# Optimization experiments

Measured on AMD Instinct MI355X. Metric: run time of the kernel, lower is better.

The kernel has to match this reference:

```python
import jax, jax.numpy as jnp
import numpy as np

B, T, NX, NXS, H, NY, NYS = 16384, 60, 4, 3, 64, 4, 3


def _lstm(x, h0, c0, Wih, Whh, bih, bhh):
    """PyTorch-convention LSTM (gate order i,f,g,o). x: [B,T,X]. Returns (hs [B,T,H], hT, cT)."""
    # precompute input contribution for all timesteps: [T,B,4H]
    xg = jnp.transpose(jnp.einsum('btx,gx->btg', x, Wih) + (bih + bhh), (1, 0, 2))

    def step(carry, xg_t):
        h, c = carry
        g = xg_t + h @ Whh.T
        i, f, gg, o = jnp.split(g, 4, axis=-1)
        c = jax.nn.sigmoid(f) * c + jax.nn.sigmoid(i) * jnp.tanh(gg)
        h = jax.nn.sigmoid(o) * jnp.tanh(c)
        return (h, c), h

    (hT, cT), hs = jax.lax.scan(step, (h0, c0), xg)
    return jnp.transpose(hs, (1, 0, 2)), hT, cT


def setup_inputs() -> dict:
    key = jax.random.key(0)
    ks = jax.random.split(key, 24)
    w = lambda k, shp: (jax.random.normal(k, shp, jnp.float32) * 0.1)
    return {
        'inputs_main': jax.random.normal(ks[0], (B, T, NX), jnp.float32),
        'inputs_aux': jax.random.normal(ks[1], (B, NXS), jnp.float32),
        'hx2': jax.random.normal(ks[2], (B, H), jnp.float32),
        'cx2': jax.random.normal(ks[3], (B, H), jnp.float32),
        'Ws1': w(ks[4], (H, NXS)), 'bs1': w(ks[5], (H,)),
        'Ws2': w(ks[6], (H, NXS)), 'bs2': w(ks[7], (H,)),
        'Wih1': w(ks[8], (4 * H, NX)), 'Whh1': w(ks[9], (4 * H, H)),
        'bih1': w(ks[10], (4 * H,)), 'bhh1': w(ks[11], (4 * H,)),
        'Wih2': w(ks[12], (4 * H, H)), 'Whh2': w(ks[13], (4 * H, H)),
        'bih2': w(ks[14], (4 * H,)), 'bhh2': w(ks[15], (4 * H,)),
        'Wlat': w(ks[16], (H, H)), 'blat': w(ks[17], (H,)),
        'Wout': w(ks[18], (NY, H)), 'bout': w(ks[19], (NY,)),
        'Wsfc': w(ks[20], (NYS, H)), 'bsfc': w(ks[21], (NYS,)),
    }


def reference(inputs_main, inputs_aux, hx2, cx2, Ws1, bs1, Ws2, bs2,
              Wih1, Whh1, bih1, bhh1, Wih2, Whh2, bih2, bhh2,
              Wlat, blat, Wout, bout, Wsfc, bsfc):
    # surface MLPs -> initial LSTM1 state (h raw, c tanh'd)
    hx = inputs_aux @ Ws1.T + bs1
    cx = jnp.tanh(inputs_aux @ Ws2.T + bs2)
    # run LSTM1 top-down (flipped levels)
    x1 = jnp.flip(inputs_main, axis=1)
    rnn1out, _, _ = _lstm(x1, hx, cx, Wih1, Whh1, bih1, bhh1)
    # flip back and run LSTM2 bottom-up with (hx2, cx2)
    # (the original calls rnn2 twice; only the second call's result is used)
    rnn1out_f = jnp.flip(rnn1out, axis=1)
    rnn2out, last_h, _ = _lstm(rnn1out_f, hx2, cx2, Wih2, Whh2, bih2, bhh2)
    # intermediate MLP + output head
    lat = rnn2out @ Wlat.T + blat                # [B,T,H]
    out = lat @ Wout.T + bout                    # [B,T,NY]
    out_sfc = jax.nn.relu(last_h @ Wsfc.T + bsfc)  # [B,NYS]
    return out, out_sfc
```

## Files before the change

### kernel.cpp

```cpp
#include <hip/hip_runtime.h>
#include <hip/hip_bf16.h>

#define BB 16384
#define TT 60

typedef short bf16x8 __attribute__((ext_vector_type(8)));
typedef float f32x4 __attribute__((ext_vector_type(4)));

__device__ __forceinline__ unsigned short f2bs(float f) {
    __hip_bfloat16 h = __float2bfloat16(f);
    return __builtin_bit_cast(unsigned short, h);
}

__device__ __forceinline__ unsigned cvtpk2(float lo, float hi) {
    unsigned r;
    asm("v_cvt_pk_bf16_f32 %0, %1, %2" : "=v"(r) : "v"(lo), "v"(hi));
    return r;
}

__device__ __forceinline__ void lstm_cell(float xi, float xf, float xg, float xo,
                                          float& c, float& h) {
    xi = __builtin_amdgcn_fmed3f(xi, -17.f, 17.f);
    xf = __builtin_amdgcn_fmed3f(xf, -17.f, 17.f);
    xo = __builtin_amdgcn_fmed3f(xo, -17.f, 17.f);
    xg = __builtin_amdgcn_fmed3f(xg, -11.f, 11.f);
    const float ei = __expf(-xi), ef = __expf(-xf), eo = __expf(-xo), eg = __expf(2.f * xg);
    const float di = 1.f + ei, df = 1.f + ef, dd = 1.f + eo, dg = 1.f + eg;
    const float a = di * df, b = dd * dg;
    const float R = __builtin_amdgcn_rcpf(a * b);
    const float si = df * b * R;
    const float sf = di * b * R;
    const float so = a * dg * R;
    const float tg = (eg - 1.f) * (a * dd) * R;
    const float cn = sf * c + si * tg;
    c = cn;
    const float tc = __builtin_amdgcn_fmed3f(cn, -11.f, 11.f);
    const float ec = __expf(2.f * tc);
    const float th = (ec - 1.f) * __builtin_amdgcn_rcpf(ec + 1.f);
    h = so * th;
}

#define STEP_BARRIER() do {                                   \
    asm volatile("s_waitcnt lgkmcnt(0)" ::: "memory");        \
    __builtin_amdgcn_s_barrier();                             \
    __builtin_amdgcn_sched_barrier(0);                        \
} while (0)

__device__ __forceinline__ bf16x8 pack8(float4 a, float4 b) {
    bf16x8 r;
    r[0] = (short)f2bs(a.x); r[1] = (short)f2bs(a.y);
    r[2] = (short)f2bs(a.z); r[3] = (short)f2bs(a.w);
    r[4] = (short)f2bs(b.x); r[5] = (short)f2bs(b.y);
    r[6] = (short)f2bs(b.z); r[7] = (short)f2bs(b.w);
    return r;
}

__global__ __launch_bounds__(256, 2) void k_lstm1(
    const float* __restrict__ xmain, const float* __restrict__ aux,
    const float* __restrict__ Ws1, const float* __restrict__ bs1,
    const float* __restrict__ Ws2, const float* __restrict__ bs2,
    const float* __restrict__ Wih1, const float* __restrict__ Whh1,
    const float* __restrict__ bih1, const float* __restrict__ bhh1,
    unsigned short* __restrict__ rnn1t)
{
    __shared__ unsigned short hB[2 * 4096];

    const int tid = threadIdx.x;
    {
        unsigned int* p32 = (unsigned int*)hB;
        #pragma unroll
        for (int e = 0; e < 16; ++e) p32[tid + 256 * e] = 0;
    }
    const int hj = tid >> 6, lane = tid & 63;
    const int row16 = lane & 15, quad = lane >> 4;
    const int b0 = blockIdx.x * 32;
    const int swz = (row16 & 7) << 3;

    bf16x8 wf[4][3];
    float fb[4];
    #pragma unroll
    for (int i = 0; i < 4; ++i) {
        const int g = (hj + 4 * i) * 16 + row16;
        const float* wr = Whh1 + g * 64 + quad * 8;
        wf[i][0] = pack8(*(const float4*)wr, *(const float4*)(wr + 4));
        wf[i][1] = pack8(*(const float4*)(wr + 32), *(const float4*)(wr + 36));
        float4 z4 = {0.f, 0.f, 0.f, 0.f};
        float4 xw = z4;
        if (quad == 0) xw = *(const float4*)(Wih1 + g * 4);
        wf[i][2] = pack8(xw, z4);
        fb[i] = bih1[g] + bhh1[g];
    }
    __syncthreads();

    const int j = hj * 16 + row16;
    const unsigned oA0 = (unsigned)(((row16 * 128 + 0 + quad * 8) ^ swz) * 2);
    const unsigned oA1 = (unsigned)(((row16 * 128 + 32 + quad * 8) ^ swz) * 2);
    const unsigned oA2 = (unsigned)(((row16 * 128 + 64 + quad * 8) ^ swz) * 2);
    unsigned oW[4];
    #pragma unroll
    for (int r = 0; r < 4; ++r) {
        const int m = quad * 4 + r;
        oW[r] = (unsigned)(((m * 128 + j) ^ ((m & 7) << 3)) * 2);
    }
    const unsigned oX = (unsigned)(((lane * 128 + 64) ^ ((lane & 7) << 3)) * 2);
    char* const hBb = (char*)hB;

    const float w10 = Ws1[j * 3], w11 = Ws1[j * 3 + 1], w12 = Ws1[j * 3 + 2], sb1v = bs1[j];
    const float w20 = Ws2[j * 3], w21 = Ws2[j * 3 + 1], w22 = Ws2[j * 3 + 2], sb2v = bs2[j];
    f32x4 cc[2];
    #pragma unroll
    for (int mh = 0; mh < 2; ++mh) {
        #pragma unroll
        for (int r = 0; r < 4; ++r) {
            const int m = mh * 16 + quad * 4 + r;
            const float a0v = aux[(b0 + m) * 3], a1v = aux[(b0 + m) * 3 + 1], a2v = aux[(b0 + m) * 3 + 2];
            float h0 = w10 * a0v + w11 * a1v + w12 * a2v + sb1v;
            float c0in = w20 * a0v + w21 * a1v + w22 * a2v + sb2v;
            c0in = __builtin_amdgcn_fmed3f(c0in, -11.f, 11.f);
            const float e0 = __expf(2.f * c0in);
            cc[mh][r] = (e0 - 1.f) * __builtin_amdgcn_rcpf(e0 + 1.f);
            *(unsigned short*)(hBb + oW[r] + mh * 4096) = f2bs(h0);
        }
    }
    if (hj == 2 && lane < 32) {
        float4 xv = ((const float4*)xmain)[(size_t)(b0 + lane) * TT + 59];
        uint2 p2 = { cvtpk2(xv.x, xv.y), cvtpk2(xv.z, xv.w) };
        *(uint2*)(hBb + oX) = p2;
    }
    __syncthreads();

    const float4* px = (const float4*)xmain + (size_t)(b0 + lane) * TT + 58;
    unsigned short* pst = rnn1t + ((size_t)60 * BB + b0 + ((hj >> 1) << 4) + row16) * 64 + ((hj & 1) << 5) + quad * 8;

    unsigned pofs = 0;
    #pragma unroll 1
    for (int s = 0; s < TT; ++s) {
        char* hbP = hBb + pofs;
        char* hbN = hBb + (pofs ^ 8192);
        float4 xv;
        if (hj == 2 && lane < 32 && s < TT - 1) xv = *px;
        bf16x8 a0[2], a1[2], a2[2];
        #pragma unroll
        for (int mh = 0; mh < 2; ++mh) {
            a0[mh] = *(const bf16x8*)(hbP + oA0 + mh * 4096);
            a1[mh] = *(const bf16x8*)(hbP + oA1 + mh * 4096);
            a2[mh] = *(const bf16x8*)(hbP + oA2 + mh * 4096);
        }
        if (s > 0) {
            bf16x8 sv = (hj == 0) ? a0[0] : (hj == 1) ? a1[0] : (hj == 2) ? a0[1] : a1[1];
            *(bf16x8*)pst = sv;
        }
        pst -= (size_t)BB * 64;
        px -= 1;

        f32x4 ac[2][4];
        #pragma unroll
        for (int mh = 0; mh < 2; ++mh)
            #pragma unroll
            for (int i = 0; i < 4; ++i) { f32x4 v = {fb[i], fb[i], fb[i], fb[i]}; ac[mh][i] = v; }
        #pragma unroll
        for (int mh = 0; mh < 2; ++mh) {
            #pragma unroll
            for (int i = 0; i < 4; ++i) {
                ac[mh][i] = __builtin_amdgcn_mfma_f32_16x16x32_bf16(a0[mh], wf[i][0], ac[mh][i], 0, 0, 0);
                ac[mh][i] = __builtin_amdgcn_mfma_f32_16x16x32_bf16(a1[mh], wf[i][1], ac[mh][i], 0, 0, 0);
                ac[mh][i] = __builtin_amdgcn_mfma_f32_16x16x32_bf16(a2[mh], wf[i][2], ac[mh][i], 0, 0, 0);
            }
        }
        #pragma unroll
        for (int mh = 0; mh < 2; ++mh) {
            float hr[4];
            #pragma unroll
            for (int r = 0; r < 4; ++r) {
                float cr = cc[mh][r];
                lstm_cell(ac[mh][0][r], ac[mh][1][r], ac[mh][2][r], ac[mh][3][r], cr, hr[r]);
                cc[mh][r] = cr;
            }
            const unsigned u01 = cvtpk2(hr[0], hr[1]);
            const unsigned u23 = cvtpk2(hr[2], hr[3]);
            *(unsigned short*)(hbN + oW[0] + mh * 4096) = (unsigned short)u01;
            *(unsigned short*)(hbN + oW[1] + mh * 4096) = (unsigned short)(u01 >> 16);
            *(unsigned short*)(hbN + oW[2] + mh * 4096) = (unsigned short)u23;
            *(unsigned short*)(hbN + oW[3] + mh * 4096) = (unsigned short)(u23 >> 16);
        }
        if (hj == 2 && lane < 32 && s < TT - 1) {
            uint2 p2 = { cvtpk2(xv.x, xv.y), cvtpk2(xv.z, xv.w) };
            *(uint2*)(hbN + oX) = p2;
        }
        STEP_BARRIER();
        pofs ^= 8192;
    }
    {
        char* hbP = hBb + pofs;
        bf16x8 sv;
        if (hj == 0)      sv = *(const bf16x8*)(hbP + oA0);
        else if (hj == 1) sv = *(const bf16x8*)(hbP + oA1);
        else if (hj == 2) sv = *(const bf16x8*)(hbP + oA0 + 4096);
        else              sv = *(const bf16x8*)(hbP + oA1 + 4096);
        *(bf16x8*)&rnn1t[((size_t)(b0 + ((hj >> 1) << 4) + row16)) * 64 + ((hj & 1) << 5) + quad * 8] = sv;
    }
}

__global__ __launch_bounds__(256, 2) void k_lstm2(
    const unsigned short* __restrict__ rnn1t,
    const float* __restrict__ hx2, const float* __restrict__ cx2,
    const float* __restrict__ Wih2, const float* __restrict__ Whh2,
    const float* __restrict__ bih2, const float* __restrict__ bhh2,
    const float* __restrict__ Wlat, const float* __restrict__ blat,
    const float* __restrict__ Wout, const float* __restrict__ bout,
    const float* __restrict__ Wsfc, const float* __restrict__ bsfc,
    float* __restrict__ out)
{
    __shared__ unsigned short hB[2 * 4096];
    __shared__ unsigned short whead[16 * 64];

    const int tid = threadIdx.x;
    {
        unsigned int* w32 = (unsigned int*)whead;
        w32[tid] = 0; w32[tid + 256] = 0;
    }
    const int hj = tid >> 6, lane = tid & 63;
    const int row16 = lane & 15, quad = lane >> 4;
    const int b0 = blockIdx.x * 32;
    const int swz = (row16 & 7) << 3;

    bf16x8 wf[4][4];
    float fb[4];
    #pragma unroll
    for (int i = 0; i < 4; ++i) {
        const int g = (hj + 4 * i) * 16 + row16;
        const float* wh = Whh2 + g * 64 + quad * 8;
        const float* wi = Wih2 + g * 64 + quad * 8;
        wf[i][0] = pack8(*(const float4*)wh, *(const float4*)(wh + 4));
        wf[i][1] = pack8(*(const float4*)(wh + 32), *(const float4*)(wh + 36));
        wf[i][2] = pack8(*(const float4*)wi, *(const float4*)(wi + 4));
        wf[i][3] = pack8(*(const float4*)(wi + 32), *(const float4*)(wi + 36));
        fb[i] = bih2[g] + bhh2[g];
    }
    float bcomb = 0.f;
    if (row16 < 4) {
        float s = 0.f;
        for (int jj = 0; jj < 64; ++jj) s += Wout[row16 * 64 + jj] * blat[jj];
        bcomb = s + bout[row16];
    } else if (row16 < 7) {
        bcomb = bsfc[row16 - 4];
    }
    __syncthreads();

    {
        const int o = tid >> 6, k = tid & 63;
        float s = 0.f;
        for (int jj = 0; jj < 64; ++jj) s += Wout[o * 64 + jj] * Wlat[jj * 64 + k];
        whead[(o * 64 + k) ^ ((o & 7) << 3)] = f2bs(s);
        if (tid < 192) {
            const int o2 = o + 4;
            whead[(o2 * 64 + k) ^ ((o2 & 7) << 3)] = f2bs(Wsfc[o * 64 + k]);
        }
    }

    const int j = hj * 16 + row16;
    const unsigned oA0 = (unsigned)(((row16 * 128 + 0 + quad * 8) ^ swz) * 2);
    const unsigned oA1 = (unsigned)(((row16 * 128 + 32 + quad * 8) ^ swz) * 2);
    const unsigned oA2 = (unsigned)(((row16 * 128 + 64 + quad * 8) ^ swz) * 2);
    const unsigned oA3 = (unsigned)(((row16 * 128 + 96 + quad * 8) ^ swz) * 2);
    unsigned oW[4];
    #pragma unroll
    for (int r = 0; r < 4; ++r) {
        const int m = quad * 4 + r;
        oW[r] = (unsigned)(((m * 128 + j) ^ ((m & 7) << 3)) * 2);
    }
    const unsigned oPV = (unsigned)(((row16 * 128 + 64 + ((hj & 1) << 5) + quad * 8) ^ swz) * 2);
    const unsigned oH0 = (unsigned)(((row16 * 64 + 0 + quad * 8) ^ swz) * 2);
    const unsigned oH1 = (unsigned)(((row16 * 64 + 32 + quad * 8) ^ swz) * 2);
    char* const hBb = (char*)hB;
    char* const whb = (char*)whead;

    f32x4 cc[2];
    #pragma unroll
    for (int mh = 0; mh < 2; ++mh) {
        #pragma unroll
        for (int r = 0; r < 4; ++r) {
            const int m = mh * 16 + quad * 4 + r;
            cc[mh][r] = cx2[(size_t)(b0 + m) * 64 + j];
            *(unsigned short*)(hBb + oW[r] + mh * 4096) = f2bs(hx2[(size_t)(b0 + m) * 64 + j]);
        }
    }
    if (hj < 2) {
        bf16x8 v0 = *(const bf16x8*)&rnn1t[((size_t)(b0 + row16)) * 64 + ((hj & 1) << 5) + quad * 8];
        bf16x8 v1 = *(const bf16x8*)&rnn1t[((size_t)(b0 + 16 + row16)) * 64 + ((hj & 1) << 5) + quad * 8];
        *(bf16x8*)(hBb + oPV) = v0;
        *(bf16x8*)(hBb + oPV + 4096) = v1;
    }
    __syncthreads();

    bf16x8 wh0 = *(const bf16x8*)(whb + oH0);
    bf16x8 wh1 = *(const bf16x8*)(whb + oH1);

    const unsigned short* ppv = rnn1t + ((size_t)BB + b0 + row16) * 64 + ((hj & 1) << 5) + quad * 8;
    float* po = out + ((size_t)(b0 + ((hj == 2) ? 16 : 0) + quad * 4) * TT) * 4 + row16;

    unsigned pofs = 0;
    #pragma unroll 1
    for (int t = 0; t < TT; ++t) {
        char* hbP = hBb + pofs;
        char* hbN = hBb + (pofs ^ 8192);
        bf16x8 pv0, pv1;
        if (hj < 2 && t < TT - 1) {
            pv0 = *(const bf16x8*)ppv;
            pv1 = *(const bf16x8*)(ppv + 16 * 64);
        }
        ppv += (size_t)BB * 64;

        bf16x8 a0[2], a1[2], a2[2], a3[2];
        #pragma unroll
        for (int mh = 0; mh < 2; ++mh) {
            a0[mh] = *(const bf16x8*)(hbP + oA0 + mh * 4096);
            a1[mh] = *(const bf16x8*)(hbP + oA1 + mh * 4096);
            a2[mh] = *(const bf16x8*)(hbP + oA2 + mh * 4096);
            a3[mh] = *(const bf16x8*)(hbP + oA3 + mh * 4096);
        }

        if (hj >= 2 && t > 0) {
            const bf16x8 ha0 = (hj == 3) ? a0[0] : a0[1];
            const bf16x8 ha1 = (hj == 3) ? a1[0] : a1[1];
            f32x4 hacc = {bcomb, bcomb, bcomb, bcomb};
            hacc = __builtin_amdgcn_mfma_f32_16x16x32_bf16(ha0, wh0, hacc, 0, 0, 0);
            hacc = __builtin_amdgcn_mfma_f32_16x16x32_bf16(ha1, wh1, hacc, 0, 0, 0);
            if (row16 < 4) {
                #pragma unroll
                for (int r = 0; r < 4; ++r)
                    po[r * TT * 4] = hacc[r];
            }
            po += 4;
        }

        f32x4 ac[2][4];
        #pragma unroll
        for (int mh = 0; mh < 2; ++mh)
            #pragma unroll
            for (int i = 0; i < 4; ++i) { f32x4 v = {fb[i], fb[i], fb[i], fb[i]}; ac[mh][i] = v; }
        #pragma unroll
        for (int mh = 0; mh < 2; ++mh) {
            #pragma unroll
            for (int i = 0; i < 4; ++i) {
                ac[mh][i] = __builtin_amdgcn_mfma_f32_16x16x32_bf16(a0[mh], wf[i][0], ac[mh][i], 0, 0, 0);
                ac[mh][i] = __builtin_amdgcn_mfma_f32_16x16x32_bf16(a1[mh], wf[i][1], ac[mh][i], 0, 0, 0);
                ac[mh][i] = __builtin_amdgcn_mfma_f32_16x16x32_bf16(a2[mh], wf[i][2], ac[mh][i], 0, 0, 0);
                ac[mh][i] = __builtin_amdgcn_mfma_f32_16x16x32_bf16(a3[mh], wf[i][3], ac[mh][i], 0, 0, 0);
            }
        }
        #pragma unroll
        for (int mh = 0; mh < 2; ++mh) {
            float hr[4];
            #pragma unroll
            for (int r = 0; r < 4; ++r) {
                float cr = cc[mh][r];
                lstm_cell(ac[mh][0][r], ac[mh][1][r], ac[mh][2][r], ac[mh][3][r], cr, hr[r]);
                cc[mh][r] = cr;
            }
            const unsigned u01 = cvtpk2(hr[0], hr[1]);
            const unsigned u23 = cvtpk2(hr[2], hr[3]);
            *(unsigned short*)(hbN + oW[0] + mh * 4096) = (unsigned short)u01;
            *(unsigned short*)(hbN + oW[1] + mh * 4096) = (unsigned short)(u01 >> 16);
            *(unsigned short*)(hbN + oW[2] + mh * 4096) = (unsigned short)u23;
            *(unsigned short*)(hbN + oW[3] + mh * 4096) = (unsigned short)(u23 >> 16);
        }
        if (hj < 2 && t < TT - 1) {
            *(bf16x8*)(hbN + oPV) = pv0;
            *(bf16x8*)(hbN + oPV + 4096) = pv1;
        }
        STEP_BARRIER();
        pofs ^= 8192;
    }
    if (hj >= 2) {
        char* hbP = hBb + pofs;
        const int mho = (hj == 3) ? 0 : 4096;
        bf16x8 ea0 = *(const bf16x8*)(hbP + oA0 + mho);
        bf16x8 ea1 = *(const bf16x8*)(hbP + oA1 + mho);
        f32x4 hacc = {bcomb, bcomb, bcomb, bcomb};
        hacc = __builtin_amdgcn_mfma_f32_16x16x32_bf16(ea0, wh0, hacc, 0, 0, 0);
        hacc = __builtin_amdgcn_mfma_f32_16x16x32_bf16(ea1, wh1, hacc, 0, 0, 0);
        const int rb = b0 + ((hj == 2) ? 16 : 0) + quad * 4;
        if (row16 < 4) {
            #pragma unroll
            for (int r = 0; r < 4; ++r)
                out[((size_t)(rb + r) * TT + 59) * 4 + row16] = hacc[r];
        } else if (row16 < 7) {
            float* osfc = out + (size_t)BB * TT * 4;
            #pragma unroll
            for (int r = 0; r < 4; ++r)
                osfc[(size_t)(rb + r) * 3 + (row16 - 4)] = fmaxf(hacc[r], 0.f);
        }
    }
}

extern "C" void kernel_launch(void* const* d_in, const int* in_sizes, int n_in,
                              void* d_out, int out_size, void* d_ws, size_t ws_size,
                              hipStream_t stream) {
    const float* xmain = (const float*)d_in[0];
    const float* aux   = (const float*)d_in[1];
    const float* hx2   = (const float*)d_in[2];
    const float* cx2   = (const float*)d_in[3];
    const float* Ws1   = (const float*)d_in[4];
    const float* bs1   = (const float*)d_in[5];
    const float* Ws2   = (const float*)d_in[6];
    const float* bs2   = (const float*)d_in[7];
    const float* Wih1  = (const float*)d_in[8];
    const float* Whh1  = (const float*)d_in[9];
    const float* bih1  = (const float*)d_in[10];
    const float* bhh1  = (const float*)d_in[11];
    const float* Wih2  = (const float*)d_in[12];
    const float* Whh2  = (const float*)d_in[13];
    const float* bih2  = (const float*)d_in[14];
    const float* bhh2  = (const float*)d_in[15];
    const float* Wlat  = (const float*)d_in[16];
    const float* blat  = (const float*)d_in[17];
    const float* Wout  = (const float*)d_in[18];
    const float* bout  = (const float*)d_in[19];
    const float* Wsfc  = (const float*)d_in[20];
    const float* bsfc  = (const float*)d_in[21];

    unsigned short* rnn1t = (unsigned short*)d_ws;
    float* out = (float*)d_out;

    dim3 grid(BB / 32), block(256);
    k_lstm1<<<grid, block, 0, stream>>>(xmain, aux, Ws1, bs1, Ws2, bs2,
                                        Wih1, Whh1, bih1, bhh1, rnn1t);
    k_lstm2<<<grid, block, 0, stream>>>(rnn1t, hx2, cx2, Wih2, Whh2, bih2, bhh2,
                                        Wlat, blat, Wout, bout, Wsfc, bsfc, out);
}
```

Before: 237.6 us.

## Fold exp2 scaling into LSTM weights and split LSTM2 h/x LDS buffers

Multiplies the recurrent and input weights and biases by -log2(e) (or 2·log2(e) for the g gate) at load time, so the cell can call exp2 directly without negating or scaling the pre-activations. The clamp bounds are rescaled to match. In LSTM2, the shared h-state buffer is split into separate h2 and h1 buffers, and every wave now prefetches one rnn1 row-slice per step instead of two waves each loading two. The m-half loop is also made non-unrolled, which lowers register pressure but serialises MFMA and activation work across the two halves. Folding the scale into bf16 weights shifts rounding slightly.

```diff
diff --git a/kernel.cpp b/kernel.cpp
--- a/kernel.cpp
+++ b/kernel.cpp
@@ -3,6 +3,7 @@
 
 #define BB 16384
 #define TT 60
+#define L2E 1.44269504089f
 
 typedef short bf16x8 __attribute__((ext_vector_type(8)));
 typedef float f32x4 __attribute__((ext_vector_type(4)));
@@ -18,13 +19,14 @@
     return r;
 }
 
-__device__ __forceinline__ void lstm_cell(float xi, float xf, float xg, float xo,
+__device__ __forceinline__ void lstm_cell(float yi, float yf, float yg, float yo,
                                           float& c, float& h) {
-    xi = __builtin_amdgcn_fmed3f(xi, -17.f, 17.f);
-    xf = __builtin_amdgcn_fmed3f(xf, -17.f, 17.f);
-    xo = __builtin_amdgcn_fmed3f(xo, -17.f, 17.f);
-    xg = __builtin_amdgcn_fmed3f(xg, -11.f, 11.f);
-    const float ei = __expf(-xi), ef = __expf(-xf), eo = __expf(-xo), eg = __expf(2.f * xg);
+    yi = __builtin_amdgcn_fmed3f(yi, -24.53f, 24.53f);
+    yf = __builtin_amdgcn_fmed3f(yf, -24.53f, 24.53f);
+    yo = __builtin_amdgcn_fmed3f(yo, -24.53f, 24.53f);
+    yg = __builtin_amdgcn_fmed3f(yg, -31.74f, 31.74f);
+    const float ei = __builtin_exp2f(yi), ef = __builtin_exp2f(yf);
+    const float eo = __builtin_exp2f(yo), eg = __builtin_exp2f(yg);
     const float di = 1.f + ei, df = 1.f + ef, dd = 1.f + eo, dg = 1.f + eg;
     const float a = di * df, b = dd * dg;
     const float R = __builtin_amdgcn_rcpf(a * b);
@@ -35,7 +37,7 @@
     const float cn = sf * c + si * tg;
     c = cn;
     const float tc = __builtin_amdgcn_fmed3f(cn, -11.f, 11.f);
-    const float ec = __expf(2.f * tc);
+    const float ec = __builtin_exp2f(2.f * L2E * tc);
     const float th = (ec - 1.f) * __builtin_amdgcn_rcpf(ec + 1.f);
     h = so * th;
 }
@@ -46,12 +48,12 @@
     __builtin_amdgcn_sched_barrier(0);                        \
 } while (0)
 
-__device__ __forceinline__ bf16x8 pack8(float4 a, float4 b) {
+__device__ __forceinline__ bf16x8 pack8s(float4 a, float4 b, float s) {
     bf16x8 r;
-    r[0] = (short)f2bs(a.x); r[1] = (short)f2bs(a.y);
-    r[2] = (short)f2bs(a.z); r[3] = (short)f2bs(a.w);
-    r[4] = (short)f2bs(b.x); r[5] = (short)f2bs(b.y);
-    r[6] = (short)f2bs(b.z); r[7] = (short)f2bs(b.w);
+    r[0] = (short)f2bs(a.x * s); r[1] = (short)f2bs(a.y * s);
+    r[2] = (short)f2bs(a.z * s); r[3] = (short)f2bs(a.w * s);
+    r[4] = (short)f2bs(b.x * s); r[5] = (short)f2bs(b.y * s);
+    r[6] = (short)f2bs(b.z * s); r[7] = (short)f2bs(b.w * s);
     return r;
 }
 
@@ -76,19 +78,22 @@
     const int b0 = blockIdx.x * 32;
     const int swz = (row16 & 7) << 3;
 
+    const float gs = (hj == 2) ? (2.f * L2E) : (-L2E);
+    (void)gs;
     bf16x8 wf[4][3];
     float fb[4];
     #pragma unroll
     for (int i = 0; i < 4; ++i) {
+        const float s = (i == 2) ? (2.f * L2E) : (-L2E);
         const int g = (hj + 4 * i) * 16 + row16;
         const float* wr = Whh1 + g * 64 + quad * 8;
-        wf[i][0] = pack8(*(const float4*)wr, *(const float4*)(wr + 4));
-        wf[i][1] = pack8(*(const float4*)(wr + 32), *(const float4*)(wr + 36));
+        wf[i][0] = pack8s(*(const float4*)wr, *(const float4*)(wr + 4), s);
+        wf[i][1] = pack8s(*(const float4*)(wr + 32), *(const float4*)(wr + 36), s);
         float4 z4 = {0.f, 0.f, 0.f, 0.f};
         float4 xw = z4;
         if (quad == 0) xw = *(const float4*)(Wih1 + g * 4);
-        wf[i][2] = pack8(xw, z4);
-        fb[i] = bih1[g] + bhh1[g];
+        wf[i][2] = pack8s(xw, z4, s);
+        fb[i] = (bih1[g] + bhh1[g]) * s;
     }
     __syncthreads();
 
@@ -117,7 +122,7 @@
             float h0 = w10 * a0v + w11 * a1v + w12 * a2v + sb1v;
             float c0in = w20 * a0v + w21 * a1v + w22 * a2v + sb2v;
             c0in = __builtin_amdgcn_fmed3f(c0in, -11.f, 11.f);
-            const float e0 = __expf(2.f * c0in);
+            const float e0 = __builtin_exp2f(2.f * L2E * c0in);
             cc[mh][r] = (e0 - 1.f) * __builtin_amdgcn_rcpf(e0 + 1.f);
             *(unsigned short*)(hBb + oW[r] + mh * 4096) = f2bs(h0);
         }
@@ -211,7 +216,8 @@
     const float* __restrict__ Wsfc, const float* __restrict__ bsfc,
     float* __restrict__ out)
 {
-    __shared__ unsigned short hB[2 * 4096];
+    __shared__ unsigned short h2B[2 * 2048];
+    __shared__ unsigned short h1B[2 * 2048];
     __shared__ unsigned short whead[16 * 64];
 
     const int tid = threadIdx.x;
@@ -228,20 +234,21 @@
     float fb[4];
     #pragma unroll
     for (int i = 0; i < 4; ++i) {
+        const float s = (i == 2) ? (2.f * L2E) : (-L2E);
         const int g = (hj + 4 * i) * 16 + row16;
         const float* wh = Whh2 + g * 64 + quad * 8;
         const float* wi = Wih2 + g * 64 + quad * 8;
-        wf[i][0] = pack8(*(const float4*)wh, *(const float4*)(wh + 4));
-        wf[i][1] = pack8(*(const float4*)(wh + 32), *(const float4*)(wh + 36));
-        wf[i][2] = pack8(*(const float4*)wi, *(const float4*)(wi + 4));
-        wf[i][3] = pack8(*(const float4*)(wi + 32), *(const float4*)(wi + 36));
-        fb[i] = bih2[g] + bhh2[g];
+        wf[i][0] = pack8s(*(const float4*)wh, *(const float4*)(wh + 4), s);
+        wf[i][1] = pack8s(*(const float4*)(wh + 32), *(const float4*)(wh + 36), s);
+        wf[i][2] = pack8s(*(const float4*)wi, *(const float4*)(wi + 4), s);
+        wf[i][3] = pack8s(*(const float4*)(wi + 32), *(const float4*)(wi + 36), s);
+        fb[i] = (bih2[g] + bhh2[g]) * s;
     }
     float bcomb = 0.f;
     if (row16 < 4) {
-        float s = 0.f;
-        for (int jj = 0; jj < 64; ++jj) s += Wout[row16 * 64 + jj] * blat[jj];
-        bcomb = s + bout[row16];
+        float ss = 0.f;
+        for (int jj = 0; jj < 64; ++jj) ss += Wout[row16 * 64 + jj] * blat[jj];
+        bcomb = ss + bout[row16];
     } else if (row16 < 7) {
         bcomb = bsfc[row16 - 4];
     }
@@ -249,9 +256,9 @@
 
     {
         const int o = tid >> 6, k = tid & 63;
-        float s = 0.f;
-        for (int jj = 0; jj < 64; ++jj) s += Wout[o * 64 + jj] * Wlat[jj * 64 + k];
-        whead[(o * 64 + k) ^ ((o & 7) << 3)] = f2bs(s);
+        float ss = 0.f;
+        for (int jj = 0; jj < 64; ++jj) ss += Wout[o * 64 + jj] * Wlat[jj * 64 + k];
+        whead[(o * 64 + k) ^ ((o & 7) << 3)] = f2bs(ss);
         if (tid < 192) {
             const int o2 = o + 4;
             whead[(o2 * 64 + k) ^ ((o2 & 7) << 3)] = f2bs(Wsfc[o * 64 + k]);
@@ -259,20 +266,19 @@
     }
 
     const int j = hj * 16 + row16;
-    const unsigned oA0 = (unsigned)(((row16 * 128 + 0 + quad * 8) ^ swz) * 2);
-    const unsigned oA1 = (unsigned)(((row16 * 128 + 32 + quad * 8) ^ swz) * 2);
-    const unsigned oA2 = (unsigned)(((row16 * 128 + 64 + quad * 8) ^ swz) * 2);
-    const unsigned oA3 = (unsigned)(((row16 * 128 + 96 + quad * 8) ^ swz) * 2);
+    const unsigned oA0 = (unsigned)(((row16 * 64 + 0 + quad * 8) ^ swz) * 2);
+    const unsigned oA1 = (unsigned)(((row16 * 64 + 32 + quad * 8) ^ swz) * 2);
     unsigned oW[4];
     #pragma unroll
     for (int r = 0; r < 4; ++r) {
         const int m = quad * 4 + r;
-        oW[r] = (unsigned)(((m * 128 + j) ^ ((m & 7) << 3)) * 2);
-    }
-    const unsigned oPV = (unsigned)(((row16 * 128 + 64 + ((hj & 1) << 5) + quad * 8) ^ swz) * 2);
+        oW[r] = (unsigned)(((m * 64 + j) ^ ((m & 7) << 3)) * 2);
+    }
+    const unsigned oPV = (unsigned)((hj >> 1) * 2048 + (((row16 * 64 + ((hj & 1) << 5) + quad * 8) ^ swz) * 2));
     const unsigned oH0 = (unsigned)(((row16 * 64 + 0 + quad * 8) ^ swz) * 2);
     const unsigned oH1 = (unsigned)(((row16 * 64 + 32 + quad * 8) ^ swz) * 2);
-    char* const hBb = (char*)hB;
+    char* const h2Bb = (char*)h2B;
+    char* const h1Bb = (char*)h1B;
     char* const whb = (char*)whead;
 
     f32x4 cc[2];
@@ -282,101 +288,86 @@
         for (int r = 0; r < 4; ++r) {
             const int m = mh * 16 + quad * 4 + r;
             cc[mh][r] = cx2[(size_t)(b0 + m) * 64 + j];
-            *(unsigned short*)(hBb + oW[r] + mh * 4096) = f2bs(hx2[(size_t)(b0 + m) * 64 + j]);
-        }
-    }
-    if (hj < 2) {
-        bf16x8 v0 = *(const bf16x8*)&rnn1t[((size_t)(b0 + row16)) * 64 + ((hj & 1) << 5) + quad * 8];
-        bf16x8 v1 = *(const bf16x8*)&rnn1t[((size_t)(b0 + 16 + row16)) * 64 + ((hj & 1) << 5) + quad * 8];
-        *(bf16x8*)(hBb + oPV) = v0;
-        *(bf16x8*)(hBb + oPV + 4096) = v1;
+            *(unsigned short*)(h2Bb + oW[r] + mh * 2048) = f2bs(hx2[(size_t)(b0 + m) * 64 + j]);
+        }
+    }
+    const unsigned short* pbase = rnn1t + ((size_t)(b0 + ((hj >> 1) << 4) + row16)) * 64 + ((hj & 1) << 5) + quad * 8;
+    {
+        bf16x8 v = *(const bf16x8*)pbase;
+        *(bf16x8*)(h1Bb + oPV) = v;
     }
     __syncthreads();
 
     bf16x8 wh0 = *(const bf16x8*)(whb + oH0);
     bf16x8 wh1 = *(const bf16x8*)(whb + oH1);
 
-    const unsigned short* ppv = rnn1t + ((size_t)BB + b0 + row16) * 64 + ((hj & 1) << 5) + quad * 8;
+    const unsigned short* ppv = pbase + (size_t)BB * 64;
     float* po = out + ((size_t)(b0 + ((hj == 2) ? 16 : 0) + quad * 4) * TT) * 4 + row16;
 
     unsigned pofs = 0;
     #pragma unroll 1
     for (int t = 0; t < TT; ++t) {
-        char* hbP = hBb + pofs;
-        char* hbN = hBb + (pofs ^ 8192);
-        bf16x8 pv0, pv1;
-        if (hj < 2 && t < TT - 1) {
-            pv0 = *(const bf16x8*)ppv;
-            pv1 = *(const bf16x8*)(ppv + 16 * 64);
-        }
+        char* hbP2 = h2Bb + pofs;
+        char* hbN2 = h2Bb + (pofs ^ 4096);
+        char* hbP1 = h1Bb + pofs;
+        char* hbN1 = h1Bb + (pofs ^ 4096);
+        bf16x8 pv;
+        if (t < TT - 1) pv = *(const bf16x8*)ppv;
         ppv += (size_t)BB * 64;
 
-        bf16x8 a0[2], a1[2], a2[2], a3[2];
-        #pragma unroll
+        #pragma unroll 1
         for (int mh = 0; mh < 2; ++mh) {
-            a0[mh] = *(const bf16x8*)(hbP + oA0 + mh * 4096);
-            a1[mh] = *(const bf16x8*)(hbP + oA1 + mh * 4096);
-            a2[mh] = *(const bf16x8*)(hbP + oA2 + mh * 4096);
-            a3[mh] = *(const bf16x8*)(hbP + oA3 + mh * 4096);
-        }
-
-        if (hj >= 2 && t > 0) {
-            const bf16x8 ha0 = (hj == 3) ? a0[0] : a0[1];
-            const bf16x8 ha1 = (hj == 3) ? a1[0] : a1[1];
-            f32x4 hacc = {bcomb, bcomb, bcomb, bcomb};
-            hacc = __builtin_amdgcn_mfma_f32_16x16x32_bf16(ha0, wh0, hacc, 0, 0, 0);
-            hacc = __builtin_amdgcn_mfma_f32_16x16x32_bf16(ha1, wh1, hacc, 0, 0, 0);
-            if (row16 < 4) {
-                #pragma unroll
-                for (int r = 0; r < 4; ++r)
-                    po[r * TT * 4] = hacc[r];
+            const int mo = mh * 2048;
+            bf16x8 a0 = *(const bf16x8*)(hbP2 + oA0 + mo);
+            bf16x8 a1 = *(const bf16x8*)(hbP2 + oA1 + mo);
+            bf16x8 a2 = *(const bf16x8*)(hbP1 + oA0 + mo);
+            bf16x8 a3 = *(const bf16x8*)(hbP1 + oA1 + mo);
+
+            if (t > 0 && hj == 3 - mh) {
+                f32x4 hacc = {bcomb, bcomb, bcomb, bcomb};
+                hacc = __builtin_amdgcn_mfma_f32_16x16x32_bf16(a0, wh0, hacc, 0, 0, 0);
+                hacc = __builtin_amdgcn_mfma_f32_16x16x32_bf16(a1, wh1, hacc, 0, 0, 0);
+                if (row16 < 4) {
+                    #pragma unroll
+                    for (int r = 0; r < 4; ++r)
+                        po[r * TT * 4] = hacc[r];
+                }
+                po += 4;
             }
-            po += 4;
-        }
-
-        f32x4 ac[2][4];
-        #pragma unroll
-        for (int mh = 0; mh < 2; ++mh)
-            #pragma unroll
-            for (int i = 0; i < 4; ++i) { f32x4 v = {fb[i], fb[i], fb[i], fb[i]}; ac[mh][i] = v; }
-        #pragma unroll
-        for (int mh = 0; mh < 2; ++mh) {
+
+            f32x4 ac[4];
+            #pragma unroll
+            for (int i = 0; i < 4; ++i) { f32x4 v = {fb[i], fb[i], fb[i], fb[i]}; ac[i] = v; }
             #pragma unroll
             for (int i = 0; i < 4; ++i) {
-                ac[mh][i] = __builtin_amdgcn_mfma_f32_16x16x32_bf16(a0[mh], wf[i][0], ac[mh][i], 0, 0, 0);
-                ac[mh][i] = __builtin_amdgcn_mfma_f32_16x16x32_bf16(a1[mh], wf[i][1], ac[mh][i], 0, 0, 0);
-                ac[mh][i] = __builtin_amdgcn_mfma_f32_16x16x32_bf16(a2[mh], wf[i][2], ac[mh][i], 0, 0, 0);
-                ac[mh][i] = __builtin_amdgcn_mfma_f32_16x16x32_bf16(a3[mh], wf[i][3], ac[mh][i], 0, 0, 0);
+                ac[i] = __builtin_amdgcn_mfma_f32_16x16x32_bf16(a0, wf[i][0], ac[i], 0, 0, 0);
+                ac[i] = __builtin_amdgcn_mfma_f32_16x16x32_bf16(a1, wf[i][1], ac[i], 0, 0, 0);
+                ac[i] = __builtin_amdgcn_mfma_f32_16x16x32_bf16(a2, wf[i][2], ac[i], 0, 0, 0);
+                ac[i] = __builtin_amdgcn_mfma_f32_16x16x32_bf16(a3, wf[i][3], ac[i], 0, 0, 0);
             }
-        }
-        #pragma unroll
-        for (int mh = 0; mh < 2; ++mh) {
             float hr[4];
             #pragma unroll
             for (int r = 0; r < 4; ++r) {
                 float cr = cc[mh][r];
-                lstm_cell(ac[mh][0][r], ac[mh][1][r], ac[mh][2][r], ac[mh][3][r], cr, hr[r]);
+                lstm_cell(ac[0][r], ac[1][r], ac[2][r], ac[3][r], cr, hr[r]);
                 cc[mh][r] = cr;
             }
             const unsigned u01 = cvtpk2(hr[0], hr[1]);
             const unsigned u23 = cvtpk2(hr[2], hr[3]);
-            *(unsigned short*)(hbN + oW[0] + mh * 4096) = (unsigned short)u01;
-            *(unsigned short*)(hbN + oW[1] + mh * 4096) = (unsigned short)(u01 >> 16);
-            *(unsigned short*)(hbN + oW[2] + mh * 4096) = (unsigned short)u23;
-            *(unsigned short*)(hbN + oW[3] + mh * 4096) = (unsigned short)(u23 >> 16);
-        }
-        if (hj < 2 && t < TT - 1) {
-            *(bf16x8*)(hbN + oPV) = pv0;
-            *(bf16x8*)(hbN + oPV + 4096) = pv1;
-        }
+            *(unsigned short*)(hbN2 + oW[0] + mo) = (unsigned short)u01;
+            *(unsigned short*)(hbN2 + oW[1] + mo) = (unsigned short)(u01 >> 16);
+            *(unsigned short*)(hbN2 + oW[2] + mo) = (unsigned short)u23;
+            *(unsigned short*)(hbN2 + oW[3] + mo) = (unsigned short)(u23 >> 16);
+        }
+        if (t < TT - 1) *(bf16x8*)(hbN1 + oPV) = pv;
         STEP_BARRIER();
-        pofs ^= 8192;
+        pofs ^= 4096;
     }
     if (hj >= 2) {
-        char* hbP = hBb + pofs;
-        const int mho = (hj == 3) ? 0 : 4096;
-        bf16x8 ea0 = *(const bf16x8*)(hbP + oA0 + mho);
-        bf16x8 ea1 = *(const bf16x8*)(hbP + oA1 + mho);
+        char* hbP2 = h2Bb + pofs;
+        const int mho = (hj == 3) ? 0 : 2048;
+        bf16x8 ea0 = *(const bf16x8*)(hbP2 + oA0 + mho);
+        bf16x8 ea1 = *(const bf16x8*)(hbP2 + oA1 + mho);
         f32x4 hacc = {bcomb, bcomb, bcomb, bcomb};
         hacc = __builtin_amdgcn_mfma_f32_16x16x32_bf16(ea0, wh0, hacc, 0, 0, 0);
         hacc = __builtin_amdgcn_mfma_f32_16x16x32_bf16(ea1, wh1, hacc, 0, 0, 0);
```

After: 303.9 us. 1.28x slower.
